# Performance work log

Measured on AMD Instinct MI355X. Metric: run time of the kernel, lower is better.

The kernel has to match this reference:

```python
import jax, jax.numpy as jnp
import numpy as np

V = 100000   # input_size == output_size (item vocab)
H = 256      # hidden_size
B = 512      # batch_size
L = 1        # num_layers


def setup_inputs() -> dict:
    key = jax.random.key(0)
    k0, k1, k2, k3, k4 = jax.random.split(key, 5)
    s = 1.0 / np.sqrt(H)  # pytorch default uniform bound scale
    return {
        "input": jax.random.randint(k0, (B,), 0, V),
        "target": jax.random.randint(k1, (B,), 0, V),
        "hidden": jnp.zeros((L, B, H), jnp.float32),
        # GRU weights, pytorch gate layout [r; z; n]
        "w_ih": jax.random.uniform(k2, (3 * H, V), jnp.float32, -s, s),
        "w_hh": jax.random.uniform(k3, (3 * H, H), jnp.float32, -s, s),
        "b_ih": jnp.zeros((3 * H,), jnp.float32),
        "b_hh": jnp.zeros((3 * H,), jnp.float32),
        # h2o linear
        "w_out": jax.random.uniform(k4, (V, H), jnp.float32, -s, s),
        "b_out": jnp.zeros((V,), jnp.float32),
    }


def reference(input, target, hidden, w_ih, w_hh, b_ih, b_hh, w_out, b_out):
    # one-hot(input) @ w_ih.T is mathematically a column gather of w_ih
    h = hidden[0]                                        # (B, H)
    gi = jnp.take(w_ih, input, axis=1).T + b_ih          # (B, 3H)
    gh = h @ w_hh.T + b_hh                               # (B, 3H)
    i_r, i_z, i_n = jnp.split(gi, 3, axis=1)
    h_r, h_z, h_n = jnp.split(gh, 3, axis=1)
    r = jax.nn.sigmoid(i_r + h_r)
    z = jax.nn.sigmoid(i_z + h_z)
    n = jnp.tanh(i_n + r * h_n)
    h_new = (1.0 - z) * n + z * h                        # (B, H)
    logit = jnp.tanh(h_new @ w_out.T + b_out)            # (B, V)
    return logit, h_new[None]                            # ((B,V), (L,B,H))
```

## Files before the change

kernel.cpp:

```cpp
#include <hip/hip_runtime.h>
#include <hip/hip_bf16.h>
#include <math.h>

#define V 100000
#define H 256
#define B 512

typedef __bf16 bf16x8 __attribute__((ext_vector_type(8)));
typedef float  f32x4  __attribute__((ext_vector_type(4)));

__device__ __forceinline__ unsigned short f32_bf16_rne(float x) {
    unsigned u = __float_as_uint(x);
    u += 0x7FFFu + ((u >> 16) & 1u);
    return (unsigned short)(u >> 16);
}
__device__ __forceinline__ float bf16u_f32(unsigned short h) {
    return __uint_as_float(((unsigned)h) << 16);
}
__device__ __forceinline__ float fast_tanh(float x) {
    float e = __builtin_exp2f(x * 2.8853900817779268f);
    return 1.f - 2.f * __builtin_amdgcn_rcpf(e + 1.f);
}

#define GLOAD_LDS16(g, l)                                                     \
    __builtin_amdgcn_global_load_lds(                                         \
        (const __attribute__((address_space(1))) void*)(g),                   \
        (__attribute__((address_space(3))) void*)(l), 16, 0, 0)

#define PREP_GRID 2304

__global__ __launch_bounds__(256) void gru_and_split(
    const int*   __restrict__ input,
    const float* __restrict__ hidden,
    const float* __restrict__ w_ih,
    const float* __restrict__ w_hh,
    const float* __restrict__ b_ih,
    const float* __restrict__ b_hh,
    const float* __restrict__ w_out,
    float*       __restrict__ h_out,
    unsigned short* __restrict__ h_hi_p,
    unsigned short* __restrict__ h_lo_p,
    unsigned short* __restrict__ w_hi_p,
    unsigned short* __restrict__ w_lo_p)
{
    if (blockIdx.x >= 256) {
        const int total4 = (V * H) / 4;
        for (int i = (blockIdx.x - 256) * 256 + threadIdx.x; i < total4;
             i += 2048 * 256) {
            const float4 x = reinterpret_cast<const float4*>(w_out)[i];
            const float f[4] = {x.x, x.y, x.z, x.w};
            ushort4 hv, lv;
            unsigned short* hp = &hv.x;
            unsigned short* lp = &lv.x;
            #pragma unroll
            for (int jj = 0; jj < 4; ++jj) {
                hp[jj] = f32_bf16_rne(f[jj]);
                lp[jj] = f32_bf16_rne(f[jj] - bf16u_f32(hp[jj]));
            }
            reinterpret_cast<ushort4*>(w_hi_p)[i] = hv;
            reinterpret_cast<ushort4*>(w_lo_p)[i] = lv;
        }
        return;
    }

    const int gb  = blockIdx.x >> 2;
    const int q   = blockIdx.x & 3;
    const int b0  = gb * 8;
    const int j0  = q * 64;
    const int tid = threadIdx.x;
    const int jj  = tid & 63;
    const int bq  = tid >> 6;
    const int j   = j0 + jj;

    __shared__ float hs[8 * H];
    __shared__ int   idxs[8];
    #pragma unroll
    for (int i = 0; i < 2; ++i) {
        const int p = i * 256 + tid;
        reinterpret_cast<float4*>(hs)[p] =
            reinterpret_cast<const float4*>(hidden + (size_t)b0 * H)[p];
    }
    if (tid < 8) idxs[tid] = input[b0 + tid];
    __syncthreads();

    const int ba = bq * 2, bb = bq * 2 + 1;
    const int ia = idxs[ba], ib = idxs[bb];

    const float g_ra = w_ih[(size_t) j          * V + ia];
    const float g_rb = w_ih[(size_t) j          * V + ib];
    const float g_za = w_ih[(size_t)(j +     H) * V + ia];
    const float g_zb = w_ih[(size_t)(j +     H) * V + ib];
    const float g_na = w_ih[(size_t)(j + 2 * H) * V + ia];
    const float g_nb = w_ih[(size_t)(j + 2 * H) * V + ib];

    const float4* wr = reinterpret_cast<const float4*>(&w_hh[(size_t) j          * H]);
    const float4* wz = reinterpret_cast<const float4*>(&w_hh[(size_t)(j +     H) * H]);
    const float4* wn = reinterpret_cast<const float4*>(&w_hh[(size_t)(j + 2 * H) * H]);
    const float4* ha = reinterpret_cast<const float4*>(&hs[ba * H]);
    const float4* hb = reinterpret_cast<const float4*>(&hs[bb * H]);

    float ara = 0.f, aza = 0.f, ana = 0.f;
    float arb = 0.f, azb = 0.f, anb = 0.f;
    #pragma unroll 4
    for (int k = 0; k < H / 4; ++k) {
        const float4 a = wr[k];
        const float4 c = wz[k];
        const float4 d = wn[k];
        const float4 va = ha[k];
        const float4 vb = hb[k];
        ara += a.x * va.x + a.y * va.y + a.z * va.z + a.w * va.w;
        aza += c.x * va.x + c.y * va.y + c.z * va.z + c.w * va.w;
        ana += d.x * va.x + d.y * va.y + d.z * va.z + d.w * va.w;
        arb += a.x * vb.x + a.y * vb.y + a.z * vb.z + a.w * vb.w;
        azb += c.x * vb.x + c.y * vb.y + c.z * vb.z + c.w * vb.w;
        anb += d.x * vb.x + d.y * vb.y + d.z * vb.z + d.w * vb.w;
    }

    const float bir = b_ih[j], biz = b_ih[j + H], bin = b_ih[j + 2 * H];
    const float bhr = b_hh[j], bhz = b_hh[j + H], bhn = b_hh[j + 2 * H];

    #pragma unroll
    for (int s = 0; s < 2; ++s) {
        const float gi_r = (s ? g_rb : g_ra) + bir;
        const float gi_z = (s ? g_zb : g_za) + biz;
        const float gi_n = (s ? g_nb : g_na) + bin;
        const float h_r  = (s ? arb : ara) + bhr;
        const float h_z  = (s ? azb : aza) + bhz;
        const float h_n  = (s ? anb : ana) + bhn;
        const int   bg   = b0 + (s ? bb : ba);

        const float r = 1.f / (1.f + expf(-(gi_r + h_r)));
        const float z = 1.f / (1.f + expf(-(gi_z + h_z)));
        const float n = tanhf(gi_n + r * h_n);
        const float hprev = hs[(s ? bb : ba) * H + jj + j0];
        const float val = (1.f - z) * n + z * hprev;

        h_out[(size_t)bg * H + j] = val;
        if (h_hi_p != nullptr) {
            const unsigned short hh = f32_bf16_rne(val);
            h_hi_p[(size_t)bg * H + j] = hh;
            h_lo_p[(size_t)bg * H + j] = f32_bf16_rne(val - bf16u_f32(hh));
        }
    }
}

#define BM  64
#define BN  128
#define BK  64
#define NVB 782
#define NBB 8

__global__ __launch_bounds__(256, 4) void out_gemm_lean(
    const unsigned short* __restrict__ whi_g,
    const unsigned short* __restrict__ wlo_g,
    const unsigned short* __restrict__ hhi_g,
    const unsigned short* __restrict__ hlo_g,
    const float*          __restrict__ b_out,
    float*                __restrict__ logit)
{
    __shared__ unsigned short w_hi_s[BN * BK];
    __shared__ unsigned short w_lo_s[BN * BK];

    const int tid  = threadIdx.x;
    const int lane = tid & 63;
    const int wid  = tid >> 6;
    const int wm   = wid >> 1;
    const int wn   = wid & 1;

    const int bid = blockIdx.x;
    const int wg  = (bid & 7) * NVB + (bid >> 3);
    const int bx  = wg & 7;
    const int by  = wg >> 3;
    const int b0  = bx * BM;
    const int v0  = by * BN;

    auto stage = [&](int k0) {
        #pragma unroll
        for (int i = 0; i < 4; ++i) {
            const int p    = i * 4096 + (wid << 10) + (lane << 4);
            const int row  = p >> 7;
            const int lb   = p & 127;
            const int swz  = lb ^ ((row & 7) << 4);
            int vg = v0 + row; if (vg > V - 1) vg = V - 1;
            const size_t gb = (size_t)vg * (H * 2) + (size_t)(k0 * 2) + swz;
            const int dst  = i * 4096 + (wid << 10);
            GLOAD_LDS16((const char*)whi_g + gb, (char*)w_hi_s + dst);
            GLOAD_LDS16((const char*)wlo_g + gb, (char*)w_lo_s + dst);
        }
    };

    bf16x8 ah[4], al[4];
    auto loadA = [&](int t) {
        #pragma unroll
        for (int i = 0; i < 2; ++i) {
            #pragma unroll
            for (int ks = 0; ks < 2; ++ks) {
                const size_t ho = ((size_t)(b0 + wm * 32 + i * 16 + (lane & 15)) * H
                                   + t * BK + ks * 32 + (lane >> 4) * 8) * 2;
                ah[i * 2 + ks] = *reinterpret_cast<const bf16x8*>(
                                     reinterpret_cast<const char*>(hhi_g) + ho);
                al[i * 2 + ks] = *reinterpret_cast<const bf16x8*>(
                                     reinterpret_cast<const char*>(hlo_g) + ho);
            }
        }
    };

    f32x4 acc[2][4];
    #pragma unroll
    for (int i = 0; i < 2; ++i)
        #pragma unroll
        for (int n = 0; n < 4; ++n)
            acc[i][n] = f32x4{0.f, 0.f, 0.f, 0.f};

    auto compute = [&]() {
        #pragma unroll
        for (int ks = 0; ks < 2; ++ks) {
            const int kb = ks * 64 + (lane >> 4) * 16;
            bf16x8 bh[4], bl[4];
            #pragma unroll
            for (int n = 0; n < 4; ++n) {
                const int row = wn * 64 + n * 16 + (lane & 15);
                const int off = row * (BK * 2) + (kb ^ ((row & 7) << 4));
                bh[n] = *reinterpret_cast<const bf16x8*>(
                            reinterpret_cast<const char*>(w_hi_s) + off);
                bl[n] = *reinterpret_cast<const bf16x8*>(
                            reinterpret_cast<const char*>(w_lo_s) + off);
            }
            #pragma unroll
            for (int n = 0; n < 4; ++n) {
                #pragma unroll
                for (int i = 0; i < 2; ++i) {
                    const bf16x8 a_h = ah[i * 2 + ks];
                    const bf16x8 a_l = al[i * 2 + ks];
                    acc[i][n] = __builtin_amdgcn_mfma_f32_16x16x32_bf16(a_h, bh[n], acc[i][n], 0, 0, 0);
                    acc[i][n] = __builtin_amdgcn_mfma_f32_16x16x32_bf16(a_h, bl[n], acc[i][n], 0, 0, 0);
                    acc[i][n] = __builtin_amdgcn_mfma_f32_16x16x32_bf16(a_l, bh[n], acc[i][n], 0, 0, 0);
                }
            }
        }
    };

    #pragma unroll
    for (int t = 0; t < 4; ++t) {
        stage(t * BK);
        loadA(t);
        __syncthreads();
        compute();
        __syncthreads();
    }

    float bias[4];
    int   cols[4];
    #pragma unroll
    for (int n = 0; n < 4; ++n) {
        const int c = v0 + wn * 64 + n * 16 + (lane & 15);
        cols[n] = c;
        bias[n] = (c < V) ? b_out[c] : 0.f;
    }
    const int rbase = b0 + wm * 32 + (lane >> 4) * 4;
    #pragma unroll
    for (int i = 0; i < 2; ++i) {
        #pragma unroll
        for (int r = 0; r < 4; ++r) {
            const int row = rbase + i * 16 + r;
            float* dst = logit + (size_t)row * V;
            #pragma unroll
            for (int n = 0; n < 4; ++n) {
                if (cols[n] < V)
                    dst[cols[n]] = fast_tanh(acc[i][n][r] + bias[n]);
            }
        }
    }
}

__global__ __launch_bounds__(256) void out_gemm_mfma_reg(
    const float* __restrict__ hnew,
    const float* __restrict__ w_out,
    const float* __restrict__ b_out,
    float*       __restrict__ logit)
{
    __shared__ unsigned short w_hi[BN * BK];
    __shared__ unsigned short w_lo[BN * BK];
    __shared__ unsigned short h_hi[BM * BK];
    __shared__ unsigned short h_lo[BM * BK];

    const int tid  = threadIdx.x;
    const int lane = tid & 63;
    const int wid  = tid >> 6;
    const int wm   = wid >> 1;
    const int wn   = wid & 1;

    const int bid = blockIdx.x;
    const int wg  = (bid & 7) * NVB + (bid >> 3);
    const int bx  = wg & 7;
    const int by  = wg >> 3;
    const int b0  = bx * BM;
    const int v0  = by * BN;

    float4 wreg[8];
    float4 hreg[4];

    auto load_chunk = [&](int k0) {
        #pragma unroll
        for (int i = 0; i < 8; ++i) {
            const int idx4 = i * 256 + tid;
            const int row  = idx4 >> 4;
            const int k4   = (idx4 & 15) << 2;
            int vg = v0 + row; if (vg > V - 1) vg = V - 1;
            wreg[i] = *reinterpret_cast<const float4*>(&w_out[(size_t)vg * H + k0 + k4]);
        }
        #pragma unroll
        for (int i = 0; i < 4; ++i) {
            const int idx4 = i * 256 + tid;
            const int row  = idx4 >> 4;
            const int k4   = (idx4 & 15) << 2;
            hreg[i] = *reinterpret_cast<const float4*>(&hnew[(b0 + row) * H + k0 + k4]);
        }
    };

    auto store_chunk = [&]() {
        #pragma unroll
        for (int i = 0; i < 8; ++i) {
            const int idx4 = i * 256 + tid;
            const int row  = idx4 >> 4;
            const int k4   = (idx4 & 15) << 2;
            const int off  = row * (BK * 2) + ((k4 * 2) ^ ((row & 7) << 4));
            const float f[4] = {wreg[i].x, wreg[i].y, wreg[i].z, wreg[i].w};
            unsigned short hv[4], lv[4];
            #pragma unroll
            for (int jj = 0; jj < 4; ++jj) {
                hv[jj] = f32_bf16_rne(f[jj]);
                lv[jj] = f32_bf16_rne(f[jj] - bf16u_f32(hv[jj]));
            }
            *reinterpret_cast<ushort4*>(reinterpret_cast<char*>(w_hi) + off) =
                make_ushort4(hv[0], hv[1], hv[2], hv[3]);
            *reinterpret_cast<ushort4*>(reinterpret_cast<char*>(w_lo) + off) =
                make_ushort4(lv[0], lv[1], lv[2], lv[3]);
        }
        #pragma unroll
        for (int i = 0; i < 4; ++i) {
            const int idx4 = i * 256 + tid;
            const int row  = idx4 >> 4;
            const int k4   = (idx4 & 15) << 2;
            const int off  = row * (BK * 2) + ((k4 * 2) ^ ((row & 7) << 4));
            const float f[4] = {hreg[i].x, hreg[i].y, hreg[i].z, hreg[i].w};
            unsigned short hv[4], lv[4];
            #pragma unroll
            for (int jj = 0; jj < 4; ++jj) {
                hv[jj] = f32_bf16_rne(f[jj]);
                lv[jj] = f32_bf16_rne(f[jj] - bf16u_f32(hv[jj]));
            }
            *reinterpret_cast<ushort4*>(reinterpret_cast<char*>(h_hi) + off) =
                make_ushort4(hv[0], hv[1], hv[2], hv[3]);
            *reinterpret_cast<ushort4*>(reinterpret_cast<char*>(h_lo) + off) =
                make_ushort4(lv[0], lv[1], lv[2], lv[3]);
        }
    };

    f32x4 acc[2][4];
    #pragma unroll
    for (int i = 0; i < 2; ++i)
        #pragma unroll
        for (int n = 0; n < 4; ++n)
            acc[i][n] = f32x4{0.f, 0.f, 0.f, 0.f};

    auto compute = [&]() {
        #pragma unroll
        for (int ks = 0; ks < 2; ++ks) {
            const int kb = ks * 64 + (lane >> 4) * 16;
            bf16x8 ah[2], al[2];
            #pragma unroll
            for (int i = 0; i < 2; ++i) {
                const int row = wm * 32 + i * 16 + (lane & 15);
                const int off = row * (BK * 2) + (kb ^ ((row & 7) << 4));
                ah[i] = *reinterpret_cast<const bf16x8*>(
                            reinterpret_cast<const char*>(h_hi) + off);
                al[i] = *reinterpret_cast<const bf16x8*>(
                            reinterpret_cast<const char*>(h_lo) + off);
            }
            #pragma unroll
            for (int n = 0; n < 4; ++n) {
                const int row = wn * 64 + n * 16 + (lane & 15);
                const int off = row * (BK * 2) + (kb ^ ((row & 7) << 4));
                const bf16x8 bh = *reinterpret_cast<const bf16x8*>(
                            reinterpret_cast<const char*>(w_hi) + off);
                const bf16x8 bl = *reinterpret_cast<const bf16x8*>(
                            reinterpret_cast<const char*>(w_lo) + off);
                #pragma unroll
                for (int i = 0; i < 2; ++i) {
                    acc[i][n] = __builtin_amdgcn_mfma_f32_16x16x32_bf16(ah[i], bh, acc[i][n], 0, 0, 0);
                    acc[i][n] = __builtin_amdgcn_mfma_f32_16x16x32_bf16(ah[i], bl, acc[i][n], 0, 0, 0);
                    acc[i][n] = __builtin_amdgcn_mfma_f32_16x16x32_bf16(al[i], bh, acc[i][n], 0, 0, 0);
                }
            }
        }
    };

    load_chunk(0);
    store_chunk();
    __syncthreads();
    for (int t = 0; t < 4; ++t) {
        if (t < 3) load_chunk((t + 1) * BK);
        compute();
        __syncthreads();
        if (t < 3) { store_chunk(); __syncthreads(); }
    }

    float bias[4];
    int   cols[4];
    #pragma unroll
    for (int n = 0; n < 4; ++n) {
        const int c = v0 + wn * 64 + n * 16 + (lane & 15);
        cols[n] = c;
        bias[n] = (c < V) ? b_out[c] : 0.f;
    }
    const int rbase = b0 + wm * 32 + (lane >> 4) * 4;
    #pragma unroll
    for (int i = 0; i < 2; ++i) {
        #pragma unroll
        for (int r = 0; r < 4; ++r) {
            const int row = rbase + i * 16 + r;
            float* dst = logit + (size_t)row * V;
            #pragma unroll
            for (int n = 0; n < 4; ++n) {
                if (cols[n] < V)
                    dst[cols[n]] = tanhf(acc[i][n][r] + bias[n]);
            }
        }
    }
}

extern "C" void kernel_launch(void* const* d_in, const int* in_sizes, int n_in,
                              void* d_out, int out_size, void* d_ws, size_t ws_size,
                              hipStream_t stream) {
    const int*   input  = (const int*)  d_in[0];
    const float* hidden = (const float*)d_in[2];
    const float* w_ih   = (const float*)d_in[3];
    const float* w_hh   = (const float*)d_in[4];
    const float* b_ih   = (const float*)d_in[5];
    const float* b_hh   = (const float*)d_in[6];
    const float* w_out  = (const float*)d_in[7];
    const float* b_out  = (const float*)d_in[8];

    float* out   = (float*)d_out;
    float* logit = out;
    float* h_new = out + (size_t)B * V;

    const size_t nw = (size_t)V * H;
    const size_t nh = (size_t)B * H;
    const size_t needed = (2 * nw + 2 * nh) * sizeof(unsigned short);

    if (ws_size >= needed) {
        unsigned short* whi = (unsigned short*)d_ws;
        unsigned short* wlo = whi + nw;
        unsigned short* hhi = wlo + nw;
        unsigned short* hlo = hhi + nh;

        gru_and_split<<<PREP_GRID, 256, 0, stream>>>(
            input, hidden, w_ih, w_hh, b_ih, b_hh, w_out,
            h_new, hhi, hlo, whi, wlo);
        out_gemm_lean<<<NVB * NBB, 256, 0, stream>>>(whi, wlo, hhi, hlo,
                                                     b_out, logit);
    } else {
        gru_and_split<<<256, 256, 0, stream>>>(
            input, hidden, w_ih, w_hh, b_ih, b_hh, w_out,
            h_new, nullptr, nullptr, nullptr, nullptr);
        out_gemm_mfma_reg<<<NVB * NBB, 256, 0, stream>>>(h_new, w_out,
                                                         b_out, logit);
    }
}
```

Before: 239.5 us.

## Fuse w_out bf16 split into persistent double-buffered output GEMM

Drops the separate pre-pass that splits w_out into bf16 hi/lo workspace arrays. The output GEMM now reads fp32 w_out directly, splits it in registers and writes it to double-buffered LDS while the MFMAs run on the other buffer. Each block now covers four consecutive 128-column V tiles and keeps all of its h fragments in registers, cutting the grid from 6256 to 1568 blocks. This avoids writing and re-reading about 100 MB of split weights. In exchange it adds VALU conversion work and register pressure inside the GEMM, at launch_bounds occupancy 2.

```diff
diff --git a/kernel.cpp b/kernel.cpp
--- a/kernel.cpp
+++ b/kernel.cpp
@@ -22,47 +22,17 @@
     return 1.f - 2.f * __builtin_amdgcn_rcpf(e + 1.f);
 }
 
-#define GLOAD_LDS16(g, l)                                                     \
-    __builtin_amdgcn_global_load_lds(                                         \
-        (const __attribute__((address_space(1))) void*)(g),                   \
-        (__attribute__((address_space(3))) void*)(l), 16, 0, 0)
-
-#define PREP_GRID 2304
-
-__global__ __launch_bounds__(256) void gru_and_split(
+__global__ __launch_bounds__(256) void gru_cell_v3(
     const int*   __restrict__ input,
     const float* __restrict__ hidden,
     const float* __restrict__ w_ih,
     const float* __restrict__ w_hh,
     const float* __restrict__ b_ih,
     const float* __restrict__ b_hh,
-    const float* __restrict__ w_out,
     float*       __restrict__ h_out,
     unsigned short* __restrict__ h_hi_p,
-    unsigned short* __restrict__ h_lo_p,
-    unsigned short* __restrict__ w_hi_p,
-    unsigned short* __restrict__ w_lo_p)
+    unsigned short* __restrict__ h_lo_p)
 {
-    if (blockIdx.x >= 256) {
-        const int total4 = (V * H) / 4;
-        for (int i = (blockIdx.x - 256) * 256 + threadIdx.x; i < total4;
-             i += 2048 * 256) {
-            const float4 x = reinterpret_cast<const float4*>(w_out)[i];
-            const float f[4] = {x.x, x.y, x.z, x.w};
-            ushort4 hv, lv;
-            unsigned short* hp = &hv.x;
-            unsigned short* lp = &lv.x;
-            #pragma unroll
-            for (int jj = 0; jj < 4; ++jj) {
-                hp[jj] = f32_bf16_rne(f[jj]);
-                lp[jj] = f32_bf16_rne(f[jj] - bf16u_f32(hp[jj]));
-            }
-            reinterpret_cast<ushort4*>(w_hi_p)[i] = hv;
-            reinterpret_cast<ushort4*>(w_lo_p)[i] = lv;
-        }
-        return;
-    }
-
     const int gb  = blockIdx.x >> 2;
     const int q   = blockIdx.x & 3;
     const int b0  = gb * 8;
@@ -144,22 +114,22 @@
     }
 }
 
-#define BM  64
-#define BN  128
-#define BK  64
-#define NVB 782
-#define NBB 8
-
-__global__ __launch_bounds__(256, 4) void out_gemm_lean(
-    const unsigned short* __restrict__ whi_g,
-    const unsigned short* __restrict__ wlo_g,
+#define BM   64
+#define BN   128
+#define BK   64
+#define NT   4
+#define NVG  196
+#define GRID2 (NVG * 8)
+
+__global__ __launch_bounds__(256, 2) void out_gemm_tiles(
+    const float*          __restrict__ w_out,
     const unsigned short* __restrict__ hhi_g,
     const unsigned short* __restrict__ hlo_g,
     const float*          __restrict__ b_out,
     float*                __restrict__ logit)
 {
-    __shared__ unsigned short w_hi_s[BN * BK];
-    __shared__ unsigned short w_lo_s[BN * BK];
+    __shared__ unsigned short w_hi_s[2][BN * BK];
+    __shared__ unsigned short w_lo_s[2][BN * BK];
 
     const int tid  = threadIdx.x;
     const int lane = tid & 63;
@@ -168,40 +138,57 @@
     const int wn   = wid & 1;
 
     const int bid = blockIdx.x;
-    const int wg  = (bid & 7) * NVB + (bid >> 3);
+    const int wg  = (bid & 7) * NVG + (bid >> 3);
+    const int vg  = wg >> 3;
     const int bx  = wg & 7;
-    const int by  = wg >> 3;
     const int b0  = bx * BM;
-    const int v0  = by * BN;
-
-    auto stage = [&](int k0) {
-        #pragma unroll
-        for (int i = 0; i < 4; ++i) {
-            const int p    = i * 4096 + (wid << 10) + (lane << 4);
-            const int row  = p >> 7;
-            const int lb   = p & 127;
-            const int swz  = lb ^ ((row & 7) << 4);
-            int vg = v0 + row; if (vg > V - 1) vg = V - 1;
-            const size_t gb = (size_t)vg * (H * 2) + (size_t)(k0 * 2) + swz;
-            const int dst  = i * 4096 + (wid << 10);
-            GLOAD_LDS16((const char*)whi_g + gb, (char*)w_hi_s + dst);
-            GLOAD_LDS16((const char*)wlo_g + gb, (char*)w_lo_s + dst);
-        }
-    };
-
-    bf16x8 ah[4], al[4];
-    auto loadA = [&](int t) {
-        #pragma unroll
-        for (int i = 0; i < 2; ++i) {
+    const int vbase = vg * (NT * BN);
+
+    bf16x8 aH[16], aL[16];
+    #pragma unroll
+    for (int t = 0; t < 4; ++t)
+        #pragma unroll
+        for (int i = 0; i < 2; ++i)
             #pragma unroll
             for (int ks = 0; ks < 2; ++ks) {
                 const size_t ho = ((size_t)(b0 + wm * 32 + i * 16 + (lane & 15)) * H
                                    + t * BK + ks * 32 + (lane >> 4) * 8) * 2;
-                ah[i * 2 + ks] = *reinterpret_cast<const bf16x8*>(
-                                     reinterpret_cast<const char*>(hhi_g) + ho);
-                al[i * 2 + ks] = *reinterpret_cast<const bf16x8*>(
-                                     reinterpret_cast<const char*>(hlo_g) + ho);
-            }
+                aH[t * 4 + i * 2 + ks] = *reinterpret_cast<const bf16x8*>(
+                                             reinterpret_cast<const char*>(hhi_g) + ho);
+                aL[t * 4 + i * 2 + ks] = *reinterpret_cast<const bf16x8*>(
+                                             reinterpret_cast<const char*>(hlo_g) + ho);
+            }
+
+    float4 wreg[8];
+    auto load_w = [&](int v0n, int k0n) {
+        #pragma unroll
+        for (int i = 0; i < 8; ++i) {
+            const int u   = i * 256 + tid;
+            const int row = u >> 4;
+            const int k4  = (u & 15) << 2;
+            int vgl = v0n + row; if (vgl > V - 1) vgl = V - 1;
+            wreg[i] = *reinterpret_cast<const float4*>(
+                          &w_out[(size_t)vgl * H + k0n + k4]);
+        }
+    };
+    auto store_w = [&](unsigned short* whi_b, unsigned short* wlo_b) {
+        #pragma unroll
+        for (int i = 0; i < 8; ++i) {
+            const int u   = i * 256 + tid;
+            const int row = u >> 4;
+            const int k4  = (u & 15) << 2;
+            const int off = row * (BK * 2) + ((k4 * 2) ^ ((row & 7) << 4));
+            const float f[4] = {wreg[i].x, wreg[i].y, wreg[i].z, wreg[i].w};
+            unsigned short hv[4], lv[4];
+            #pragma unroll
+            for (int jj = 0; jj < 4; ++jj) {
+                hv[jj] = f32_bf16_rne(f[jj]);
+                lv[jj] = f32_bf16_rne(f[jj] - bf16u_f32(hv[jj]));
+            }
+            *reinterpret_cast<ushort4*>(reinterpret_cast<char*>(whi_b) + off) =
+                make_ushort4(hv[0], hv[1], hv[2], hv[3]);
+            *reinterpret_cast<ushort4*>(reinterpret_cast<char*>(wlo_b) + off) =
+                make_ushort4(lv[0], lv[1], lv[2], lv[3]);
         }
     };
 
@@ -212,66 +199,90 @@
         for (int n = 0; n < 4; ++n)
             acc[i][n] = f32x4{0.f, 0.f, 0.f, 0.f};
 
-    auto compute = [&]() {
-        #pragma unroll
-        for (int ks = 0; ks < 2; ++ks) {
-            const int kb = ks * 64 + (lane >> 4) * 16;
-            bf16x8 bh[4], bl[4];
-            #pragma unroll
-            for (int n = 0; n < 4; ++n) {
-                const int row = wn * 64 + n * 16 + (lane & 15);
-                const int off = row * (BK * 2) + (kb ^ ((row & 7) << 4));
-                bh[n] = *reinterpret_cast<const bf16x8*>(
-                            reinterpret_cast<const char*>(w_hi_s) + off);
-                bl[n] = *reinterpret_cast<const bf16x8*>(
-                            reinterpret_cast<const char*>(w_lo_s) + off);
-            }
-            #pragma unroll
-            for (int n = 0; n < 4; ++n) {
+    load_w(vbase, 0);
+    store_w(&w_hi_s[0][0], &w_lo_s[0][0]);
+    __syncthreads();
+
+    for (int tt = 0; tt < NT; ++tt) {
+        const int v0 = vbase + tt * BN;
+        #pragma unroll
+        for (int ck = 0; ck < 4; ++ck) {
+            const bool last = (tt == NT - 1) && (ck == 3);
+
+            if (!last) {
+                const int nv0 = (ck == 3) ? v0 + BN : v0;
+                const int nk0 = (ck == 3) ? 0 : (ck + 1) * BK;
+                load_w(nv0, nk0);
+            }
+
+            {
+                const unsigned short* whc = &w_hi_s[ck & 1][0];
+                const unsigned short* wlc = &w_lo_s[ck & 1][0];
                 #pragma unroll
-                for (int i = 0; i < 2; ++i) {
-                    const bf16x8 a_h = ah[i * 2 + ks];
-                    const bf16x8 a_l = al[i * 2 + ks];
-                    acc[i][n] = __builtin_amdgcn_mfma_f32_16x16x32_bf16(a_h, bh[n], acc[i][n], 0, 0, 0);
-                    acc[i][n] = __builtin_amdgcn_mfma_f32_16x16x32_bf16(a_h, bl[n], acc[i][n], 0, 0, 0);
-                    acc[i][n] = __builtin_amdgcn_mfma_f32_16x16x32_bf16(a_l, bh[n], acc[i][n], 0, 0, 0);
+                for (int ks = 0; ks < 2; ++ks) {
+                    const int kb = ks * 64 + (lane >> 4) * 16;
+                    bf16x8 bh[4], bl[4];
+                    #pragma unroll
+                    for (int n = 0; n < 4; ++n) {
+                        const int row = wn * 64 + n * 16 + (lane & 15);
+                        const int off = row * (BK * 2) + (kb ^ ((row & 7) << 4));
+                        bh[n] = *reinterpret_cast<const bf16x8*>(
+                                    reinterpret_cast<const char*>(whc) + off);
+                        bl[n] = *reinterpret_cast<const bf16x8*>(
+                                    reinterpret_cast<const char*>(wlc) + off);
+                    }
+                    #pragma unroll
+                    for (int n = 0; n < 4; ++n)
+                        #pragma unroll
+                        for (int i = 0; i < 2; ++i) {
+                            const bf16x8 a_h = aH[ck * 4 + i * 2 + ks];
+                            const bf16x8 a_l = aL[ck * 4 + i * 2 + ks];
+                            acc[i][n] = __builtin_amdgcn_mfma_f32_16x16x32_bf16(a_h, bh[n], acc[i][n], 0, 0, 0);
+                            acc[i][n] = __builtin_amdgcn_mfma_f32_16x16x32_bf16(a_h, bl[n], acc[i][n], 0, 0, 0);
+                            acc[i][n] = __builtin_amdgcn_mfma_f32_16x16x32_bf16(a_l, bh[n], acc[i][n], 0, 0, 0);
+                        }
                 }
             }
-        }
-    };
-
-    #pragma unroll
-    for (int t = 0; t < 4; ++t) {
-        stage(t * BK);
-        loadA(t);
-        __syncthreads();
-        compute();
-        __syncthreads();
-    }
-
-    float bias[4];
-    int   cols[4];
-    #pragma unroll
-    for (int n = 0; n < 4; ++n) {
-        const int c = v0 + wn * 64 + n * 16 + (lane & 15);
-        cols[n] = c;
-        bias[n] = (c < V) ? b_out[c] : 0.f;
-    }
-    const int rbase = b0 + wm * 32 + (lane >> 4) * 4;
-    #pragma unroll
-    for (int i = 0; i < 2; ++i) {
-        #pragma unroll
-        for (int r = 0; r < 4; ++r) {
-            const int row = rbase + i * 16 + r;
-            float* dst = logit + (size_t)row * V;
-            #pragma unroll
-            for (int n = 0; n < 4; ++n) {
-                if (cols[n] < V)
-                    dst[cols[n]] = fast_tanh(acc[i][n][r] + bias[n]);
-            }
-        }
-    }
-}
+
+            if (!last)
+                store_w(&w_hi_s[(ck + 1) & 1][0], &w_lo_s[(ck + 1) & 1][0]);
+
+            if (ck == 3) {
+                float bias[4];
+                int   cols[4];
+                #pragma unroll
+                for (int n = 0; n < 4; ++n) {
+                    const int c = v0 + wn * 64 + n * 16 + (lane & 15);
+                    cols[n] = c;
+                    bias[n] = (c < V) ? b_out[c] : 0.f;
+                }
+                const int rbase = b0 + wm * 32 + (lane >> 4) * 4;
+                #pragma unroll
+                for (int i = 0; i < 2; ++i)
+                    #pragma unroll
+                    for (int r = 0; r < 4; ++r) {
+                        const int row = rbase + i * 16 + r;
+                        float* dst = logit + (size_t)row * V;
+                        #pragma unroll
+                        for (int n = 0; n < 4; ++n) {
+                            if (cols[n] < V)
+                                dst[cols[n]] = fast_tanh(acc[i][n][r] + bias[n]);
+                        }
+                    }
+                #pragma unroll
+                for (int i = 0; i < 2; ++i)
+                    #pragma unroll
+                    for (int n = 0; n < 4; ++n)
+                        acc[i][n] = f32x4{0.f, 0.f, 0.f, 0.f};
+            }
+
+            __syncthreads();
+        }
+    }
+}
+
+#define NVB 782
+#define NBB 8
 
 __global__ __launch_bounds__(256) void out_gemm_mfma_reg(
     const float* __restrict__ hnew,
@@ -306,8 +317,8 @@
             const int idx4 = i * 256 + tid;
             const int row  = idx4 >> 4;
             const int k4   = (idx4 & 15) << 2;
-            int vg = v0 + row; if (vg > V - 1) vg = V - 1;
-            wreg[i] = *reinterpret_cast<const float4*>(&w_out[(size_t)vg * H + k0 + k4]);
+            int vgl = v0 + row; if (vgl > V - 1) vgl = V - 1;
+            wreg[i] = *reinterpret_cast<const float4*>(&w_out[(size_t)vgl * H + k0 + k4]);
         }
         #pragma unroll
         for (int i = 0; i < 4; ++i) {
@@ -446,25 +457,21 @@
     float* logit = out;
     float* h_new = out + (size_t)B * V;
 
-    const size_t nw = (size_t)V * H;
     const size_t nh = (size_t)B * H;
-    const size_t needed = (2 * nw + 2 * nh) * sizeof(unsigned short);
+    const size_t needed = 2 * nh * sizeof(unsigned short);
 
     if (ws_size >= needed) {
-        unsigned short* whi = (unsigned short*)d_ws;
-        unsigned short* wlo = whi + nw;
-        unsigned short* hhi = wlo + nw;
+        unsigned short* hhi = (unsigned short*)d_ws;
         unsigned short* hlo = hhi + nh;
 
-        gru_and_split<<<PREP_GRID, 256, 0, stream>>>(
-            input, hidden, w_ih, w_hh, b_ih, b_hh, w_out,
-            h_new, hhi, hlo, whi, wlo);
-        out_gemm_lean<<<NVB * NBB, 256, 0, stream>>>(whi, wlo, hhi, hlo,
-                                                     b_out, logit);
+        gru_cell_v3<<<256, 256, 0, stream>>>(input, hidden, w_ih, w_hh,
+                                             b_ih, b_hh, h_new, hhi, hlo);
+        out_gemm_tiles<<<GRID2, 256, 0, stream>>>(w_out, hhi, hlo,
+                                                  b_out, logit);
     } else {
-        gru_and_split<<<256, 256, 0, stream>>>(
-            input, hidden, w_ih, w_hh, b_ih, b_hh, w_out,
-            h_new, nullptr, nullptr, nullptr, nullptr);
+        gru_cell_v3<<<256, 256, 0, stream>>>(input, hidden, w_ih, w_hh,
+                                             b_ih, b_hh, h_new,
+                                             nullptr, nullptr);
         out_gemm_mfma_reg<<<NVB * NBB, 256, 0, stream>>>(h_new, w_out,
                                                          b_out, logit);
     }
```

After: 381.6 us. 59.3% more time.

## Double-buffer LDS weight tiles with vmcnt waits and preload full A fragments

Applied to the files above, without the earlier changes.

Rewrites the output GEMM to double-buffer the bf16 hi/lo weight tiles in LDS. It issues the next K-chunk's global-to-LDS loads before computing the current one and synchronises with explicit vmcnt waits and raw barriers instead of __syncthreads. Each wave now owns 16 rows by all 128 columns, and the whole A fragment (h hi/lo for K=256) is loaded into registers once up front. Compute phases are raised to high priority with s_setprio. The goal is to hide global load latency behind MFMA work, at the cost of twice the LDS and more registers, which drops the occupancy hint from 4 to 2 blocks per CU.

```diff
diff --git a/kernel.cpp b/kernel.cpp
--- a/kernel.cpp
+++ b/kernel.cpp
@@ -26,6 +26,9 @@
     __builtin_amdgcn_global_load_lds(                                         \
         (const __attribute__((address_space(1))) void*)(g),                   \
         (__attribute__((address_space(3))) void*)(l), 16, 0, 0)
+
+#define WAIT_VM(N) asm volatile("s_waitcnt vmcnt(" #N ")" ::: "memory")
+#define SCHED_FENCE() __builtin_amdgcn_sched_barrier(0)
 
 #define PREP_GRID 2304
 
@@ -150,7 +153,7 @@
 #define NVB 782
 #define NBB 8
 
-__global__ __launch_bounds__(256, 4) void out_gemm_lean(
+__global__ __launch_bounds__(256, 2) void out_gemm_cnt(
     const unsigned short* __restrict__ whi_g,
     const unsigned short* __restrict__ wlo_g,
     const unsigned short* __restrict__ hhi_g,
@@ -158,14 +161,12 @@
     const float*          __restrict__ b_out,
     float*                __restrict__ logit)
 {
-    __shared__ unsigned short w_hi_s[BN * BK];
-    __shared__ unsigned short w_lo_s[BN * BK];
+    __shared__ unsigned short w_hi_s[2][BN * BK];
+    __shared__ unsigned short w_lo_s[2][BN * BK];
 
     const int tid  = threadIdx.x;
     const int lane = tid & 63;
     const int wid  = tid >> 6;
-    const int wm   = wid >> 1;
-    const int wn   = wid & 1;
 
     const int bid = blockIdx.x;
     const int wg  = (bid & 7) * NVB + (bid >> 3);
@@ -174,7 +175,22 @@
     const int b0  = bx * BM;
     const int v0  = by * BN;
 
-    auto stage = [&](int k0) {
+    bf16x8 aH[8], aL[8];
+    {
+        const int arow = b0 + wid * 16 + (lane & 15);
+        #pragma unroll
+        for (int s = 0; s < 8; ++s) {
+            const size_t ho = ((size_t)arow * H + s * 32 + (lane >> 4) * 8) * 2;
+            aH[s] = *reinterpret_cast<const bf16x8*>(
+                        reinterpret_cast<const char*>(hhi_g) + ho);
+            aL[s] = *reinterpret_cast<const bf16x8*>(
+                        reinterpret_cast<const char*>(hlo_g) + ho);
+        }
+    }
+    WAIT_VM(0);
+    SCHED_FENCE();
+
+    auto stage = [&](int buf, int k0) {
         #pragma unroll
         for (int i = 0; i < 4; ++i) {
             const int p    = i * 4096 + (wid << 10) + (lane << 4);
@@ -184,91 +200,88 @@
             int vg = v0 + row; if (vg > V - 1) vg = V - 1;
             const size_t gb = (size_t)vg * (H * 2) + (size_t)(k0 * 2) + swz;
             const int dst  = i * 4096 + (wid << 10);
-            GLOAD_LDS16((const char*)whi_g + gb, (char*)w_hi_s + dst);
-            GLOAD_LDS16((const char*)wlo_g + gb, (char*)w_lo_s + dst);
+            GLOAD_LDS16((const char*)whi_g + gb,
+                        (char*)&w_hi_s[buf][0] + dst);
+            GLOAD_LDS16((const char*)wlo_g + gb,
+                        (char*)&w_lo_s[buf][0] + dst);
         }
     };
 
-    bf16x8 ah[4], al[4];
-    auto loadA = [&](int t) {
-        #pragma unroll
-        for (int i = 0; i < 2; ++i) {
-            #pragma unroll
-            for (int ks = 0; ks < 2; ++ks) {
-                const size_t ho = ((size_t)(b0 + wm * 32 + i * 16 + (lane & 15)) * H
-                                   + t * BK + ks * 32 + (lane >> 4) * 8) * 2;
-                ah[i * 2 + ks] = *reinterpret_cast<const bf16x8*>(
-                                     reinterpret_cast<const char*>(hhi_g) + ho);
-                al[i * 2 + ks] = *reinterpret_cast<const bf16x8*>(
-                                     reinterpret_cast<const char*>(hlo_g) + ho);
-            }
-        }
+    f32x4 acc[8];
+    #pragma unroll
+    for (int n = 0; n < 8; ++n) acc[n] = f32x4{0.f, 0.f, 0.f, 0.f};
+
+    auto compute = [&](int buf, int t) {
+        __builtin_amdgcn_s_setprio(1);
+        #pragma unroll
+        for (int ks = 0; ks < 2; ++ks) {
+            const int s  = t * 2 + ks;
+            const int kb = ks * 64 + (lane >> 4) * 16;
+            const bf16x8 a_h = aH[s];
+            const bf16x8 a_l = aL[s];
+            #pragma unroll
+            for (int n = 0; n < 8; ++n) {
+                const int row = n * 16 + (lane & 15);
+                const int off = row * (BK * 2) + (kb ^ ((row & 7) << 4));
+                const bf16x8 bh = *reinterpret_cast<const bf16x8*>(
+                            reinterpret_cast<const char*>(&w_hi_s[buf][0]) + off);
+                const bf16x8 bl = *reinterpret_cast<const bf16x8*>(
+                            reinterpret_cast<const char*>(&w_lo_s[buf][0]) + off);
+                acc[n] = __builtin_amdgcn_mfma_f32_16x16x32_bf16(a_h, bh, acc[n], 0, 0, 0);
+                acc[n] = __builtin_amdgcn_mfma_f32_16x16x32_bf16(a_h, bl, acc[n], 0, 0, 0);
+                acc[n] = __builtin_amdgcn_mfma_f32_16x16x32_bf16(a_l, bh, acc[n], 0, 0, 0);
+            }
+        }
+        __builtin_amdgcn_s_setprio(0);
     };
 
-    f32x4 acc[2][4];
-    #pragma unroll
-    for (int i = 0; i < 2; ++i)
-        #pragma unroll
-        for (int n = 0; n < 4; ++n)
-            acc[i][n] = f32x4{0.f, 0.f, 0.f, 0.f};
-
-    auto compute = [&]() {
-        #pragma unroll
-        for (int ks = 0; ks < 2; ++ks) {
-            const int kb = ks * 64 + (lane >> 4) * 16;
-            bf16x8 bh[4], bl[4];
-            #pragma unroll
-            for (int n = 0; n < 4; ++n) {
-                const int row = wn * 64 + n * 16 + (lane & 15);
-                const int off = row * (BK * 2) + (kb ^ ((row & 7) << 4));
-                bh[n] = *reinterpret_cast<const bf16x8*>(
-                            reinterpret_cast<const char*>(w_hi_s) + off);
-                bl[n] = *reinterpret_cast<const bf16x8*>(
-                            reinterpret_cast<const char*>(w_lo_s) + off);
-            }
-            #pragma unroll
-            for (int n = 0; n < 4; ++n) {
-                #pragma unroll
-                for (int i = 0; i < 2; ++i) {
-                    const bf16x8 a_h = ah[i * 2 + ks];
-                    const bf16x8 a_l = al[i * 2 + ks];
-                    acc[i][n] = __builtin_amdgcn_mfma_f32_16x16x32_bf16(a_h, bh[n], acc[i][n], 0, 0, 0);
-                    acc[i][n] = __builtin_amdgcn_mfma_f32_16x16x32_bf16(a_h, bl[n], acc[i][n], 0, 0, 0);
-                    acc[i][n] = __builtin_amdgcn_mfma_f32_16x16x32_bf16(a_l, bh[n], acc[i][n], 0, 0, 0);
-                }
-            }
-        }
-    };
-
-    #pragma unroll
-    for (int t = 0; t < 4; ++t) {
-        stage(t * BK);
-        loadA(t);
-        __syncthreads();
-        compute();
-        __syncthreads();
-    }
-
-    float bias[4];
-    int   cols[4];
-    #pragma unroll
-    for (int n = 0; n < 4; ++n) {
-        const int c = v0 + wn * 64 + n * 16 + (lane & 15);
+    stage(0, 0);
+    stage(1, 64);
+    WAIT_VM(8);
+    __builtin_amdgcn_s_barrier();
+    SCHED_FENCE();
+
+    compute(0, 0);
+    SCHED_FENCE();
+    __builtin_amdgcn_s_barrier();
+    stage(0, 128);
+    WAIT_VM(8);
+    __builtin_amdgcn_s_barrier();
+    SCHED_FENCE();
+
+    compute(1, 1);
+    SCHED_FENCE();
+    __builtin_amdgcn_s_barrier();
+    stage(1, 192);
+    WAIT_VM(8);
+    __builtin_amdgcn_s_barrier();
+    SCHED_FENCE();
+
+    compute(0, 2);
+    SCHED_FENCE();
+    WAIT_VM(0);
+    __builtin_amdgcn_s_barrier();
+    SCHED_FENCE();
+
+    compute(1, 3);
+
+    float bias[8];
+    int   cols[8];
+    #pragma unroll
+    for (int n = 0; n < 8; ++n) {
+        const int c = v0 + n * 16 + (lane & 15);
         cols[n] = c;
         bias[n] = (c < V) ? b_out[c] : 0.f;
     }
-    const int rbase = b0 + wm * 32 + (lane >> 4) * 4;
-    #pragma unroll
-    for (int i = 0; i < 2; ++i) {
-        #pragma unroll
-        for (int r = 0; r < 4; ++r) {
-            const int row = rbase + i * 16 + r;
-            float* dst = logit + (size_t)row * V;
-            #pragma unroll
-            for (int n = 0; n < 4; ++n) {
-                if (cols[n] < V)
-                    dst[cols[n]] = fast_tanh(acc[i][n][r] + bias[n]);
-            }
+    const int rbase = b0 + wid * 16 + (lane >> 4) * 4;
+    #pragma unroll
+    for (int r = 0; r < 4; ++r) {
+        const int row = rbase + r;
+        float* dst = logit + (size_t)row * V;
+        #pragma unroll
+        for (int n = 0; n < 8; ++n) {
+            if (cols[n] < V)
+                dst[cols[n]] = fast_tanh(acc[n][r] + bias[n]);
         }
     }
 }
@@ -306,8 +319,8 @@
             const int idx4 = i * 256 + tid;
             const int row  = idx4 >> 4;
             const int k4   = (idx4 & 15) << 2;
-            int vg = v0 + row; if (vg > V - 1) vg = V - 1;
-            wreg[i] = *reinterpret_cast<const float4*>(&w_out[(size_t)vg * H + k0 + k4]);
+            int vgl = v0 + row; if (vgl > V - 1) vgl = V - 1;
+            wreg[i] = *reinterpret_cast<const float4*>(&w_out[(size_t)vgl * H + k0 + k4]);
         }
         #pragma unroll
         for (int i = 0; i < 4; ++i) {
@@ -459,8 +472,8 @@
         gru_and_split<<<PREP_GRID, 256, 0, stream>>>(
             input, hidden, w_ih, w_hh, b_ih, b_hh, w_out,
             h_new, hhi, hlo, whi, wlo);
-        out_gemm_lean<<<NVB * NBB, 256, 0, stream>>>(whi, wlo, hhi, hlo,
-                                                     b_out, logit);
+        out_gemm_cnt<<<NVB * NBB, 256, 0, stream>>>(whi, wlo, hhi, hlo,
+                                                    b_out, logit);
     } else {
         gru_and_split<<<256, 256, 0, stream>>>(
             input, hidden, w_ih, w_hh, b_ih, b_hh, w_out,
```

Result: slower. 269.4 us (+12.4%).
